# Kernel tuning notes

Hardware: AMD Instinct MI355X
Metric: run time of the kernel (lower is better)

The kernel has to match this reference:

```python
import jax, jax.numpy as jnp
import numpy as np

B, N, C = 8, 8192, 64
P, K = 2048, 16
C_IN = 2 * C + 6   # 134: concat(diff, center) of (feat ++ xyz)
H1, H2 = 64, 128
EPS = 1e-5


def setup_inputs() -> dict:
    key = jax.random.key(0)
    ks = jax.random.split(key, 16)
    inp = {
        "xyz": jax.random.normal(ks[0], (B, N, 3), dtype=jnp.float32),
        "feat": jax.random.normal(ks[1], (B, C, N), dtype=jnp.float32),
        # SharedMLP layer 1: 1x1 conv + BN(eval) + ReLU
        "W1": jax.random.normal(ks[2], (H1, C_IN), dtype=jnp.float32) * (1.0 / np.sqrt(C_IN)),
        "b1": jnp.zeros((H1,), dtype=jnp.float32),
        "g1": jax.random.uniform(ks[3], (H1,), minval=0.5, maxval=1.5, dtype=jnp.float32),
        "be1": jax.random.normal(ks[4], (H1,), dtype=jnp.float32) * 0.1,
        "m1": jax.random.normal(ks[5], (H1,), dtype=jnp.float32) * 0.1,
        "v1": jax.random.uniform(ks[6], (H1,), minval=0.5, maxval=1.5, dtype=jnp.float32),
        # SharedMLP layer 2
        "W2": jax.random.normal(ks[7], (H2, H1), dtype=jnp.float32) * (1.0 / np.sqrt(H1)),
        "b2": jnp.zeros((H2,), dtype=jnp.float32),
        "g2": jax.random.uniform(ks[8], (H2,), minval=0.5, maxval=1.5, dtype=jnp.float32),
        "be2": jax.random.normal(ks[9], (H2,), dtype=jnp.float32) * 0.1,
        "m2": jax.random.normal(ks[10], (H2,), dtype=jnp.float32) * 0.1,
        "v2": jax.random.uniform(ks[11], (H2,), minval=0.5, maxval=1.5, dtype=jnp.float32),
        "npoints": P,
    }
    return inp


def _mlp_layer(x, W, b, g, be, m, v):
    # x: [b,p,k,cin] -> 1x1 conv (einsum) + eval-mode BN + ReLU
    y = jnp.einsum("bpkc,oc->bpko", x, W) + b
    y = g * (y - m) * jax.lax.rsqrt(v + EPS) + be
    return jax.nn.relu(y)


def reference(xyz, feat, W1, b1, g1, be1, m1, v1, W2, b2, g2, be2, m2, v2, npoints):
    p = npoints
    # Range sampling: take first p points
    new_xyz = xyz[:, :p]                       # [b,p,3]
    feat_t = jnp.swapaxes(feat, 1, 2)          # [b,n,c]
    feat_x = jnp.concatenate([feat_t, xyz], axis=-1)   # [b,n,c+3] (use_xyz)
    new_feat_x = feat_x[:, :p]                 # [b,p,c+3]
    # KNN via squared euclidean distance, expanded form to avoid [b,p,n,3]
    sq_q = jnp.sum(new_xyz * new_xyz, axis=-1)           # [b,p]
    sq_r = jnp.sum(xyz * xyz, axis=-1)                   # [b,n]
    dots = jnp.einsum("bpd,bnd->bpn", new_xyz, xyz)      # [b,p,n]
    d2 = sq_q[:, :, None] + sq_r[:, None, :] - 2.0 * dots
    _, idx = jax.lax.top_k(-d2, K)             # [b,p,k] nearest (ascending dist)
    # Gather neighbor features: [b,p,k,c+3]
    knn_feat = jax.vmap(lambda f, i: f[i])(feat_x, idx)
    tiled = jnp.broadcast_to(new_feat_x[:, :, None, :], knn_feat.shape)
    edge = jnp.concatenate([knn_feat - tiled, tiled], axis=-1)  # [b,p,k,2c+6]
    h = _mlp_layer(edge, W1, b1, g1, be1, m1, v1)
    h = _mlp_layer(h, W2, b2, g2, be2, m2, v2)              # [b,p,k,H2]
    new_feat = jnp.swapaxes(jnp.max(h, axis=2), 1, 2)       # [b,H2,p]
    sample_idx = jnp.broadcast_to(jnp.arange(p, dtype=jnp.int32), (xyz.shape[0], p))
    return new_xyz, new_feat, sample_idx
```

## Files before the change

### kernel.cpp

```cpp
#include <hip/hip_runtime.h>
#include <hip/hip_bf16.h>

#define BB 8
#define NN 8192
#define CC 64
#define PP 2048
#define KK 16
#define H1 64
#define H2 128
#define K1PAD 160
#define K2PAD 72

typedef float  f32x4 __attribute__((ext_vector_type(4)));
typedef short  s16x8 __attribute__((ext_vector_type(8)));

#define OFF_FXT   0u
#define OFF_PTS4  17825792u
#define OFF_KNN   19922944u
#define OFF_W1P   20971520u
#define OFF_W2P   20992000u
#define OFF_C1    21010432u
#define OFF_C2    21010688u

#define FLTMAX 3.402823466e+38f

static __device__ __forceinline__ unsigned short bf16b(float v) {
    __hip_bfloat16 h = __float2bfloat16(v);
    return *reinterpret_cast<unsigned short*>(&h);
}
static __device__ __forceinline__ unsigned pk2(float a, float b) {
    return ((unsigned)bf16b(b) << 16) | (unsigned)bf16b(a);
}
#define LDS_FENCE() asm volatile("s_waitcnt lgkmcnt(0)" ::: "memory")

__global__ void k0_weights(const float* __restrict__ W1, const float* __restrict__ b1,
                           const float* __restrict__ g1, const float* __restrict__ be1,
                           const float* __restrict__ m1, const float* __restrict__ v1,
                           const float* __restrict__ W2, const float* __restrict__ b2,
                           const float* __restrict__ g2, const float* __restrict__ be2,
                           const float* __restrict__ m2, const float* __restrict__ v2,
                           unsigned short* __restrict__ w1p, unsigned short* __restrict__ w2p,
                           float* __restrict__ c1, float* __restrict__ c2) {
    int i = blockIdx.x * 256 + threadIdx.x;
    if (i < 64 * K1PAD) {
        int n = i / K1PAD, c = i - n * K1PAD;
        float s = g1[n] * rsqrtf(v1[n] + 1e-5f);
        float val = 0.f;
        if (c < 67)                 val = W1[n * 134 + c] * s;
        else if (c >= 72 && c < 139) val = W1[n * 134 + (c - 5)] * s;
        w1p[i] = bf16b(val);
    }
    int j = i - 64 * K1PAD;
    if (j >= 0 && j < 128 * K2PAD) {
        int o = j / K2PAD, k = j - o * K2PAD;
        float s = g2[o] * rsqrtf(v2[o] + 1e-5f);
        w2p[j] = bf16b((k < 64) ? W2[o * 64 + k] * s : 0.f);
    }
    int l = i - (64 * K1PAD + 128 * K2PAD);
    if (l >= 0 && l < 64) {
        float s = g1[l] * rsqrtf(v1[l] + 1e-5f);
        c1[l] = s * (b1[l] - m1[l]) + be1[l];
    }
    int p = l - 64;
    if (p >= 0 && p < 128) {
        float s = g2[p] * rsqrtf(v2[p] + 1e-5f);
        c2[p] = s * (b2[p] - m2[p]) + be2[p];
    }
}

__global__ __launch_bounds__(512) void k1_prep(const float* __restrict__ xyz,
                                               const float* __restrict__ feat,
                                               float* __restrict__ fxt,
                                               float4* __restrict__ pts4,
                                               float* __restrict__ out0,
                                               float* __restrict__ out2) {
    __shared__ float tile[68][65];
    int b  = blockIdx.x >> 7;
    int n0 = (blockIdx.x & 127) * 64;
    int tx = threadIdx.x & 63, ty = threadIdx.x >> 6;
    for (int c = ty; c < 68; c += 8) {
        float v;
        if (c < 64)       v = feat[((size_t)b * 64 + c) * NN + n0 + tx];
        else if (c < 67)  v = xyz[((size_t)b * NN + n0 + tx) * 3 + (c - 64)];
        else              v = 0.f;
        tile[c][tx] = v;
    }
    __syncthreads();
    size_t base = ((size_t)b * NN + n0) * 68;
    for (int e = threadIdx.x; e < 64 * 68; e += 512) {
        int nl = e / 68, c = e - nl * 68;
        fxt[base + e] = tile[c][nl];
    }
    if (threadIdx.x < 64) {
        int n = n0 + threadIdx.x;
        float x = tile[64][threadIdx.x], y = tile[65][threadIdx.x], z = tile[66][threadIdx.x];
        pts4[(size_t)b * NN + n] = make_float4(x, y, z, x * x + y * y + z * z);
        if (n0 < PP) out2[b * PP + n] = (float)n;
    }
    if (n0 < PP) {
        for (int e = threadIdx.x; e < 64 * 3; e += 512) {
            int nl = e / 3, d = e - nl * 3;
            out0[((size_t)b * PP + n0 + nl) * 3 + d] = tile[64 + d][nl];
        }
    }
}

__global__ __launch_bounds__(1024, 2) void k2_knn(const float4* __restrict__ pts4,
                                                  int* __restrict__ knn) {
    __shared__ float4 stage[8192];
    __shared__ float2 scratch[16][2][64];
    int lane = threadIdx.x & 63;
    int wv   = threadIdx.x >> 6;
    int b    = blockIdx.x >> 5;
    int q0   = (blockIdx.x & 31) * 64 + wv * 4;
    size_t pb = (size_t)b * NN;

    float4 qc = make_float4(0.f, 0.f, 0.f, 0.f);
    if (lane < 4) qc = pts4[pb + q0 + lane];
    float qx2 = -2.f * qc.x, qy2 = -2.f * qc.y, qz2 = -2.f * qc.z;
    float bx[4], by[4], bz[4];
#pragma unroll
    for (int q = 0; q < 4; ++q) {
        bx[q] = __shfl(qx2, q); by[q] = __shfl(qy2, q); bz[q] = __shfl(qz2, q);
    }

#pragma unroll
    for (int i = 0; i < 8; ++i) {
        int p = i * 1024 + threadIdx.x;
        float4 v = pts4[pb + p];
        int r = p >> 6, c = p & 63;
        stage[(r << 6) | ((c + (r >> 1)) & 63)] = v;
    }
    __syncthreads();

    float m[4];
#pragma unroll
    for (int q = 0; q < 4; ++q) m[q] = FLTMAX;
#pragma unroll
    for (int rr = 0; rr < 2; ++rr) {
        int rowbase = (2 * lane + rr) << 6;
#pragma unroll
        for (int j8 = 0; j8 < 8; ++j8) {
            float4 cc[8];
#pragma unroll
            for (int i = 0; i < 8; ++i)
                cc[i] = stage[rowbase | ((j8 * 8 + i + lane) & 63)];
#pragma unroll
            for (int q = 0; q < 4; ++q) {
                float x = bx[q], y = by[q], z = bz[q];
#pragma unroll
                for (int i = 0; i < 8; i += 2) {
                    float e0 = fmaf(z, cc[i].z, fmaf(y, cc[i].y, fmaf(x, cc[i].x, cc[i].w)));
                    float e1 = fmaf(z, cc[i+1].z, fmaf(y, cc[i+1].y, fmaf(x, cc[i+1].x, cc[i+1].w)));
                    m[q] = fminf(fminf(m[q], e0), e1);
                }
            }
        }
    }

    float sv0 = m[0], sv1 = m[1], sv2 = m[2], sv3 = m[3];
#pragma unroll
    for (int k = 2; k <= 64; k <<= 1) {
#pragma unroll
        for (int j = k >> 1; j > 0; j >>= 1) {
            bool keepMin = (((lane & k) == 0) == ((lane & j) == 0));
            float p0 = __shfl_xor(sv0, j, 64);
            float p1 = __shfl_xor(sv1, j, 64);
            float p2 = __shfl_xor(sv2, j, 64);
            float p3 = __shfl_xor(sv3, j, 64);
            sv0 = keepMin ? fminf(sv0, p0) : fmaxf(sv0, p0);
            sv1 = keepMin ? fminf(sv1, p1) : fmaxf(sv1, p1);
            sv2 = keepMin ? fminf(sv2, p2) : fmaxf(sv2, p2);
            sv3 = keepMin ? fminf(sv3, p3) : fmaxf(sv3, p3);
        }
    }
    float T[4];
    T[0] = __shfl(sv0, 15, 64); T[1] = __shfl(sv1, 15, 64);
    T[2] = __shfl(sv2, 15, 64); T[3] = __shfl(sv3, 15, 64);

    unsigned long long below = (lane == 63) ? 0x7FFFFFFFFFFFFFFFull
                                            : ((1ull << lane) - 1ull);
#pragma unroll
    for (int pr = 0; pr < 4; pr += 2) {
        int Ms[2];
#pragma unroll
        for (int u = 0; u < 2; ++u) {
            int q = pr + u;
            float x = bx[q], y = by[q], z = bz[q], tq = T[q];
            unsigned long long rm = __ballot(m[q] <= tq);
            int cnt = 0;
            while (rm) {
                int sl = __ffsll((long long)rm) - 1; rm &= rm - 1;
                int phys = (lane + sl) & 63;
                float4 c0 = stage[((2 * sl) << 6) | phys];
                float4 c1 = stage[((2 * sl + 1) << 6) | phys];
                float e0 = fmaf(z, c0.z, fmaf(y, c0.y, fmaf(x, c0.x, c0.w)));
                float e1 = fmaf(z, c1.z, fmaf(y, c1.y, fmaf(x, c1.x, c1.w)));
                unsigned long long b0 = __ballot(e0 <= tq);
                if (e0 <= tq) {
                    int pos = cnt + __popcll(b0 & below);
                    if (pos < 64)
                        scratch[wv][u][pos] = make_float2(e0, __int_as_float(sl * 128 + lane));
                }
                cnt += __popcll(b0);
                unsigned long long b1 = __ballot(e1 <= tq);
                if (e1 <= tq) {
                    int pos = cnt + __popcll(b1 & below);
                    if (pos < 64)
                        scratch[wv][u][pos] = make_float2(e1, __int_as_float(sl * 128 + 64 + lane));
                }
                cnt += __popcll(b1);
            }
            Ms[u] = min(cnt, 64);
        }
        LDS_FENCE();
#pragma unroll
        for (int u = 0; u < 2; ++u) {
            int M = Ms[u];
            float2 own = scratch[wv][u][lane];
            float di = own.x; int ni = __float_as_int(own.y);
            int rank = 0;
            const float2* buf = &scratch[wv][u][0];
#pragma unroll 4
            for (int j = 0; j < M; ++j) {
                float2 e = buf[j];
                int nj = __float_as_int(e.y);
                rank += (e.x < di || (e.x == di && nj < ni)) ? 1 : 0;
            }
            if (lane < M && rank < 16)
                knn[((size_t)(b * PP + q0 + pr + u)) * KK + rank] = ni;
        }
        LDS_FENCE();
    }
}

__global__ __launch_bounds__(256, 2) void k3_mlp(const float* __restrict__ fxt,
                                                 const int* __restrict__ knn,
                                                 const unsigned short* __restrict__ w1p,
                                                 const unsigned short* __restrict__ w2p,
                                                 const float* __restrict__ c1,
                                                 const float* __restrict__ c2,
                                                 float* __restrict__ out1) {
    __shared__ __align__(16) char smem[4 * 5632];
    __shared__ float otile[16][132];
    __shared__ __align__(16) unsigned short w1lds[64 * 168];
    int lane = threadIdx.x & 63;
    int wv   = threadIdx.x >> 6;
    int b    = blockIdx.x & 7;
    int qg   = blockIdx.x >> 3;
    int qbase = qg * 16;
    char* seg = smem + wv * 5632;
    float4* sh_t4 = (float4*)(seg + 5120);
    unsigned* sh_tbd = (unsigned*)(seg + 5392);
    unsigned short* h1l = (unsigned short*)(seg);
    const float4* fx4 = (const float4*)fxt;

    int col = lane & 15, quad = lane >> 4;
    int r = lane >> 2, s = lane & 3;

    {
        const unsigned* src = (const unsigned*)w1p;
        unsigned* dst = (unsigned*)w1lds;
        for (int t = threadIdx.x; t < 5120; t += 256) {
            int row = t / 80, c = t - row * 80;
            dst[row * 84 + c] = src[t];
        }
    }

    s16x8 w2f[2][8];
#pragma unroll
    for (int ks = 0; ks < 2; ++ks)
#pragma unroll
        for (int nt = 0; nt < 8; ++nt)
            w2f[ks][nt] = *(const s16x8*)(w2p + (nt * 16 + col) * K2PAD + ks * 32 + quad * 8);
    float c1v[4], c2v[8];
#pragma unroll
    for (int nt = 0; nt < 4; ++nt) c1v[nt] = c1[nt * 16 + col];
#pragma unroll
    for (int nt = 0; nt < 8; ++nt) c2v[nt] = c2[nt * 16 + col];

    int idxAll = knn[((size_t)(b * PP + qbase + wv * 4)) * KK + lane];

    __syncthreads();

    float4 cc[2][5];
    float4 tv[2];

#define PREFETCH(buf, qi_) {                                                  \
        int q_ = qbase + wv * 4 + (qi_);                                      \
        tv[buf] = make_float4(0.f, 0.f, 0.f, 0.f);                            \
        if (lane < 17) tv[buf] = fx4[((size_t)b * NN + q_) * 17 + lane];      \
        int nidx_ = __shfl(idxAll, (qi_) * 16 + r, 64);                       \
        const float4* rowp_ = fx4 + ((size_t)b * NN + nidx_) * 17;            \
        cc[buf][0] = rowp_[s];      cc[buf][1] = rowp_[4 + s];                \
        cc[buf][2] = rowp_[8 + s];  cc[buf][3] = rowp_[12 + s];               \
        cc[buf][4] = rowp_[16]; }

    PREFETCH(0, 0);

#pragma unroll
    for (int qi = 0; qi < 4; ++qi) {
        int cur = qi & 1, nxt = cur ^ 1;
        if (lane < 17) {
            float4 v = tv[cur];
            sh_t4[lane] = v;
            sh_tbd[lane * 2]     = pk2(v.x, v.y);
            sh_tbd[lane * 2 + 1] = pk2(v.z, v.w);
        }
        LDS_FENCE();
        char* erow = seg + r * 320;
#pragma unroll
        for (int j = 0; j < 4; ++j) {
            int c4 = j * 4 + s;
            float4 v = cc[cur][j], t = sh_t4[c4];
            *(unsigned*)(erow + c4 * 8)     = pk2(v.x - t.x, v.y - t.y);
            *(unsigned*)(erow + c4 * 8 + 4) = pk2(v.z - t.z, v.w - t.w);
        }
        if (s == 0) {
            float4 v = cc[cur][4], t = sh_t4[16];
            *(unsigned*)(erow + 128) = pk2(v.x - t.x, v.y - t.y);
            *(unsigned*)(erow + 132) = pk2(v.z - t.z, v.w - t.w);
        }
        for (int j = s; j < 34; j += 4)
            *(unsigned*)(erow + 144 + j * 4) = sh_tbd[j];
#pragma unroll
        for (int i = lane; i < 192; i += 64) {
            int rr = i / 12, jj = i - rr * 12;
            int dw = (jj < 2) ? (34 + jj) : (68 + jj);
            *(unsigned*)(seg + rr * 320 + dw * 4) = 0u;
        }
        if (qi < 3) PREFETCH(nxt, qi + 1);
        LDS_FENCE();
        f32x4 acc1[4];
#pragma unroll
        for (int nt = 0; nt < 4; ++nt) acc1[nt] = (f32x4){0.f, 0.f, 0.f, 0.f};
#pragma unroll
        for (int ks = 0; ks < 5; ++ks) {
            s16x8 a = *(const s16x8*)(seg + col * 320 + ks * 64 + quad * 16);
#pragma unroll
            for (int nt = 0; nt < 4; ++nt) {
                s16x8 bf = *(const s16x8*)(w1lds + (nt * 16 + col) * 168 + ks * 32 + quad * 8);
                acc1[nt] = __builtin_amdgcn_mfma_f32_16x16x32_bf16(a, bf, acc1[nt], 0, 0, 0);
            }
        }
#pragma unroll
        for (int nt = 0; nt < 4; ++nt) {
#pragma unroll
            for (int rr = 0; rr < 4; ++rr) {
                float y = fmaxf(acc1[nt][rr] + c1v[nt], 0.f);
                h1l[(quad * 4 + rr) * K2PAD + nt * 16 + col] = bf16b(y);
            }
        }
        {
            int rr = lane >> 2, dd = lane & 3;
            *(unsigned*)(seg + rr * 144 + 128 + dd * 4) = 0u;
        }
        LDS_FENCE();
        f32x4 acc2[8];
#pragma unroll
        for (int nt = 0; nt < 8; ++nt) acc2[nt] = (f32x4){0.f, 0.f, 0.f, 0.f};
#pragma unroll
        for (int ks = 0; ks < 2; ++ks) {
            s16x8 a = *(const s16x8*)(seg + col * 144 + ks * 64 + quad * 16);
#pragma unroll
            for (int nt = 0; nt < 8; ++nt)
                acc2[nt] = __builtin_amdgcn_mfma_f32_16x16x32_bf16(a, w2f[ks][nt], acc2[nt], 0, 0, 0);
        }
#pragma unroll
        for (int nt = 0; nt < 8; ++nt) {
            float m0 = fmaxf(fmaxf(acc2[nt][0], acc2[nt][1]), fmaxf(acc2[nt][2], acc2[nt][3]));
            m0 = m0 + c2v[nt];
            m0 = fmaxf(m0, 0.f);
            m0 = fmaxf(m0, __shfl_xor(m0, 16, 64));
            m0 = fmaxf(m0, __shfl_xor(m0, 32, 64));
            if (quad == 0)
                otile[wv * 4 + qi][nt * 16 + col] = m0;
        }
        LDS_FENCE();
    }
    __syncthreads();
    for (int i = threadIdx.x; i < H2 * 16; i += 256) {
        int ch = i >> 4, q = i & 15;
        out1[((size_t)(b * H2 + ch)) * PP + qbase + q] = otile[q][ch];
    }
#undef PREFETCH
}

extern "C" void kernel_launch(void* const* d_in, const int* in_sizes, int n_in,
                              void* d_out, int out_size, void* d_ws, size_t ws_size,
                              hipStream_t stream) {
    const float* xyz  = (const float*)d_in[0];
    const float* feat = (const float*)d_in[1];
    const float* W1   = (const float*)d_in[2];
    const float* b1   = (const float*)d_in[3];
    const float* g1   = (const float*)d_in[4];
    const float* be1  = (const float*)d_in[5];
    const float* m1   = (const float*)d_in[6];
    const float* v1   = (const float*)d_in[7];
    const float* W2   = (const float*)d_in[8];
    const float* b2   = (const float*)d_in[9];
    const float* g2   = (const float*)d_in[10];
    const float* be2  = (const float*)d_in[11];
    const float* m2   = (const float*)d_in[12];
    const float* v2   = (const float*)d_in[13];

    char* ws = (char*)d_ws;
    float*          fxt  = (float*)(ws + OFF_FXT);
    float4*         pts4 = (float4*)(ws + OFF_PTS4);
    int*            knn  = (int*)(ws + OFF_KNN);
    unsigned short* w1p  = (unsigned short*)(ws + OFF_W1P);
    unsigned short* w2p  = (unsigned short*)(ws + OFF_W2P);
    float*          c1   = (float*)(ws + OFF_C1);
    float*          c2   = (float*)(ws + OFF_C2);

    float* out0 = (float*)d_out;
    float* out1 = out0 + (size_t)BB * PP * 3;
    float* out2 = out1 + (size_t)BB * H2 * PP;

    hipLaunchKernelGGL(k0_weights, dim3(77), dim3(256), 0, stream,
                       W1, b1, g1, be1, m1, v1, W2, b2, g2, be2, m2, v2,
                       w1p, w2p, c1, c2);
    hipLaunchKernelGGL(k1_prep, dim3(1024), dim3(512), 0, stream,
                       xyz, feat, fxt, pts4, out0, out2);
    hipLaunchKernelGGL(k2_knn, dim3(256), dim3(1024), 0, stream, pts4, knn);
    hipLaunchKernelGGL(k3_mlp, dim3(1024), dim3(256), 0, stream,
                       fxt, knn, w1p, w2p, c1, c2, out1);
}
```

Measured before the change: 169.1 us.

## Split KNN candidate rows across wave pairs and fuse weight prep into prep kernel

The KNN kernel now has each pair of waves share 8 queries instead of each wave owning 4. Each wave scans half the candidate rows, the two partial top-16 thresholds are merged through LDS, and survivors are appended to a shared buffer of up to 128 entries using LDS atomics. Ranking is then split between the two waves. The weight-folding kernel is merged into the prep kernel as one extra block, removing a launch. The change adds block-wide barriers and atomic contention. The tighter combined threshold or the 128-entry cap could also change behaviour with many ties.

Result: slower. 210.9 us (+24.7%).

```diff
diff --git a/kernel.cpp b/kernel.cpp
--- a/kernel.cpp
+++ b/kernel.cpp
@@ -33,47 +33,47 @@
 }
 #define LDS_FENCE() asm volatile("s_waitcnt lgkmcnt(0)" ::: "memory")
 
-__global__ void k0_weights(const float* __restrict__ W1, const float* __restrict__ b1,
-                           const float* __restrict__ g1, const float* __restrict__ be1,
-                           const float* __restrict__ m1, const float* __restrict__ v1,
-                           const float* __restrict__ W2, const float* __restrict__ b2,
-                           const float* __restrict__ g2, const float* __restrict__ be2,
-                           const float* __restrict__ m2, const float* __restrict__ v2,
-                           unsigned short* __restrict__ w1p, unsigned short* __restrict__ w2p,
-                           float* __restrict__ c1, float* __restrict__ c2) {
-    int i = blockIdx.x * 256 + threadIdx.x;
-    if (i < 64 * K1PAD) {
-        int n = i / K1PAD, c = i - n * K1PAD;
-        float s = g1[n] * rsqrtf(v1[n] + 1e-5f);
-        float val = 0.f;
-        if (c < 67)                 val = W1[n * 134 + c] * s;
-        else if (c >= 72 && c < 139) val = W1[n * 134 + (c - 5)] * s;
-        w1p[i] = bf16b(val);
-    }
-    int j = i - 64 * K1PAD;
-    if (j >= 0 && j < 128 * K2PAD) {
-        int o = j / K2PAD, k = j - o * K2PAD;
-        float s = g2[o] * rsqrtf(v2[o] + 1e-5f);
-        w2p[j] = bf16b((k < 64) ? W2[o * 64 + k] * s : 0.f);
-    }
-    int l = i - (64 * K1PAD + 128 * K2PAD);
-    if (l >= 0 && l < 64) {
-        float s = g1[l] * rsqrtf(v1[l] + 1e-5f);
-        c1[l] = s * (b1[l] - m1[l]) + be1[l];
-    }
-    int p = l - 64;
-    if (p >= 0 && p < 128) {
-        float s = g2[p] * rsqrtf(v2[p] + 1e-5f);
-        c2[p] = s * (b2[p] - m2[p]) + be2[p];
-    }
-}
-
 __global__ __launch_bounds__(512) void k1_prep(const float* __restrict__ xyz,
                                                const float* __restrict__ feat,
+                                               const float* __restrict__ W1, const float* __restrict__ b1,
+                                               const float* __restrict__ g1, const float* __restrict__ be1,
+                                               const float* __restrict__ m1, const float* __restrict__ v1,
+                                               const float* __restrict__ W2, const float* __restrict__ b2,
+                                               const float* __restrict__ g2, const float* __restrict__ be2,
+                                               const float* __restrict__ m2, const float* __restrict__ v2,
                                                float* __restrict__ fxt,
                                                float4* __restrict__ pts4,
                                                float* __restrict__ out0,
-                                               float* __restrict__ out2) {
+                                               float* __restrict__ out2,
+                                               unsigned short* __restrict__ w1p,
+                                               unsigned short* __restrict__ w2p,
+                                               float* __restrict__ c1, float* __restrict__ c2) {
+    if (blockIdx.x >= 1024) {
+        for (int i = threadIdx.x; i < 19648; i += 512) {
+            if (i < 64 * K1PAD) {
+                int n = i / K1PAD, c = i - n * K1PAD;
+                float s = g1[n] * rsqrtf(v1[n] + 1e-5f);
+                float val = 0.f;
+                if (c < 67)                  val = W1[n * 134 + c] * s;
+                else if (c >= 72 && c < 139) val = W1[n * 134 + (c - 5)] * s;
+                w1p[i] = bf16b(val);
+            } else if (i < 19456) {
+                int j = i - 10240;
+                int o = j / K2PAD, k = j - o * K2PAD;
+                float s = g2[o] * rsqrtf(v2[o] + 1e-5f);
+                w2p[j] = bf16b((k < 64) ? W2[o * 64 + k] * s : 0.f);
+            } else if (i < 19520) {
+                int l = i - 19456;
+                float s = g1[l] * rsqrtf(v1[l] + 1e-5f);
+                c1[l] = s * (b1[l] - m1[l]) + be1[l];
+            } else {
+                int p = i - 19520;
+                float s = g2[p] * rsqrtf(v2[p] + 1e-5f);
+                c2[p] = s * (b2[p] - m2[p]) + be2[p];
+            }
+        }
+        return;
+    }
     __shared__ float tile[68][65];
     int b  = blockIdx.x >> 7;
     int n0 = (blockIdx.x & 127) * 64;
@@ -105,22 +105,28 @@
     }
 }
 
-__global__ __launch_bounds__(1024, 2) void k2_knn(const float4* __restrict__ pts4,
+__global__ __launch_bounds__(1024, 4) void k2_knn(const float4* __restrict__ pts4,
                                                   int* __restrict__ knn) {
     __shared__ float4 stage[8192];
-    __shared__ float2 scratch[16][2][64];
+    __shared__ float2 scratch[8][2][128];
+    __shared__ float  Tbuf[16][8];
+    __shared__ int    cnt[8][2];
     int lane = threadIdx.x & 63;
     int wv   = threadIdx.x >> 6;
+    int pair = wv & 7;
+    int half = wv >> 3;
     int b    = blockIdx.x >> 5;
-    int q0   = (blockIdx.x & 31) * 64 + wv * 4;
+    int q0   = (blockIdx.x & 31) * 64 + pair * 8;
     size_t pb = (size_t)b * NN;
 
+    if (threadIdx.x < 16) cnt[threadIdx.x >> 1][threadIdx.x & 1] = 0;
+
     float4 qc = make_float4(0.f, 0.f, 0.f, 0.f);
-    if (lane < 4) qc = pts4[pb + q0 + lane];
+    if (lane < 8) qc = pts4[pb + q0 + lane];
     float qx2 = -2.f * qc.x, qy2 = -2.f * qc.y, qz2 = -2.f * qc.z;
-    float bx[4], by[4], bz[4];
-#pragma unroll
-    for (int q = 0; q < 4; ++q) {
+    float bx[8], by[8], bz[8];
+#pragma unroll
+    for (int q = 0; q < 8; ++q) {
         bx[q] = __shfl(qx2, q); by[q] = __shfl(qy2, q); bz[q] = __shfl(qz2, q);
     }
 
@@ -133,104 +139,118 @@
     }
     __syncthreads();
 
-    float m[4];
-#pragma unroll
-    for (int q = 0; q < 4; ++q) m[q] = FLTMAX;
-#pragma unroll
-    for (int rr = 0; rr < 2; ++rr) {
-        int rowbase = (2 * lane + rr) << 6;
-#pragma unroll
-        for (int j8 = 0; j8 < 8; ++j8) {
-            float4 cc[8];
-#pragma unroll
-            for (int i = 0; i < 8; ++i)
-                cc[i] = stage[rowbase | ((j8 * 8 + i + lane) & 63)];
-#pragma unroll
-            for (int q = 0; q < 4; ++q) {
-                float x = bx[q], y = by[q], z = bz[q];
-#pragma unroll
-                for (int i = 0; i < 8; i += 2) {
-                    float e0 = fmaf(z, cc[i].z, fmaf(y, cc[i].y, fmaf(x, cc[i].x, cc[i].w)));
-                    float e1 = fmaf(z, cc[i+1].z, fmaf(y, cc[i+1].y, fmaf(x, cc[i+1].x, cc[i+1].w)));
-                    m[q] = fminf(fminf(m[q], e0), e1);
-                }
-            }
-        }
-    }
-
-    float sv0 = m[0], sv1 = m[1], sv2 = m[2], sv3 = m[3];
+    int row = half * 64 + lane;
+    int rowbase = row << 6;
+    float m[8];
+#pragma unroll
+    for (int q = 0; q < 8; ++q) m[q] = FLTMAX;
+#pragma unroll
+    for (int j8 = 0; j8 < 8; ++j8) {
+        float4 cc[8];
+#pragma unroll
+        for (int i = 0; i < 8; ++i)
+            cc[i] = stage[rowbase | ((j8 * 8 + i + lane) & 63)];
+#pragma unroll
+        for (int q = 0; q < 8; ++q) {
+            float x = bx[q], y = by[q], z = bz[q];
+#pragma unroll
+            for (int i = 0; i < 8; i += 2) {
+                float e0 = fmaf(z, cc[i].z, fmaf(y, cc[i].y, fmaf(x, cc[i].x, cc[i].w)));
+                float e1 = fmaf(z, cc[i+1].z, fmaf(y, cc[i+1].y, fmaf(x, cc[i+1].x, cc[i+1].w)));
+                m[q] = fminf(fminf(m[q], e0), e1);
+            }
+        }
+    }
+
+    float sv[8];
+#pragma unroll
+    for (int q = 0; q < 8; ++q) sv[q] = m[q];
 #pragma unroll
     for (int k = 2; k <= 64; k <<= 1) {
 #pragma unroll
         for (int j = k >> 1; j > 0; j >>= 1) {
             bool keepMin = (((lane & k) == 0) == ((lane & j) == 0));
-            float p0 = __shfl_xor(sv0, j, 64);
-            float p1 = __shfl_xor(sv1, j, 64);
-            float p2 = __shfl_xor(sv2, j, 64);
-            float p3 = __shfl_xor(sv3, j, 64);
-            sv0 = keepMin ? fminf(sv0, p0) : fmaxf(sv0, p0);
-            sv1 = keepMin ? fminf(sv1, p1) : fmaxf(sv1, p1);
-            sv2 = keepMin ? fminf(sv2, p2) : fmaxf(sv2, p2);
-            sv3 = keepMin ? fminf(sv3, p3) : fmaxf(sv3, p3);
-        }
-    }
-    float T[4];
-    T[0] = __shfl(sv0, 15, 64); T[1] = __shfl(sv1, 15, 64);
-    T[2] = __shfl(sv2, 15, 64); T[3] = __shfl(sv3, 15, 64);
+#pragma unroll
+            for (int q = 0; q < 8; ++q) {
+                float p = __shfl_xor(sv[q], j, 64);
+                sv[q] = keepMin ? fminf(sv[q], p) : fmaxf(sv[q], p);
+            }
+        }
+    }
+    if (lane == 0) {
+#pragma unroll
+        for (int q = 0; q < 8; ++q) Tbuf[wv][q] = 0.f;
+    }
+    float Town[8];
+#pragma unroll
+    for (int q = 0; q < 8; ++q) Town[q] = __shfl(sv[q], 15, 64);
+    if (lane == 0) {
+#pragma unroll
+        for (int q = 0; q < 8; ++q) Tbuf[wv][q] = Town[q];
+    }
+    __syncthreads();
+    float T[8];
+    unsigned long long rm[8];
+#pragma unroll
+    for (int q = 0; q < 8; ++q) {
+        T[q] = fminf(Tbuf[pair][q], Tbuf[pair + 8][q]);
+        rm[q] = __ballot(m[q] <= T[q]);
+    }
 
     unsigned long long below = (lane == 63) ? 0x7FFFFFFFFFFFFFFFull
                                             : ((1ull << lane) - 1ull);
-#pragma unroll
-    for (int pr = 0; pr < 4; pr += 2) {
-        int Ms[2];
+#pragma unroll 1
+    for (int pr = 0; pr < 8; pr += 2) {
 #pragma unroll
         for (int u = 0; u < 2; ++u) {
             int q = pr + u;
             float x = bx[q], y = by[q], z = bz[q], tq = T[q];
-            unsigned long long rm = __ballot(m[q] <= tq);
-            int cnt = 0;
-            while (rm) {
-                int sl = __ffsll((long long)rm) - 1; rm &= rm - 1;
+            unsigned long long r = rm[q];
+            while (r) {
+                int sl = __ffsll((long long)r) - 1; r &= r - 1;
+                int rw = half * 64 + sl;
                 int phys = (lane + sl) & 63;
-                float4 c0 = stage[((2 * sl) << 6) | phys];
-                float4 c1 = stage[((2 * sl + 1) << 6) | phys];
-                float e0 = fmaf(z, c0.z, fmaf(y, c0.y, fmaf(x, c0.x, c0.w)));
-                float e1 = fmaf(z, c1.z, fmaf(y, c1.y, fmaf(x, c1.x, c1.w)));
-                unsigned long long b0 = __ballot(e0 <= tq);
-                if (e0 <= tq) {
-                    int pos = cnt + __popcll(b0 & below);
-                    if (pos < 64)
-                        scratch[wv][u][pos] = make_float2(e0, __int_as_float(sl * 128 + lane));
+                float4 c = stage[(rw << 6) | phys];
+                float e = fmaf(z, c.z, fmaf(y, c.y, fmaf(x, c.x, c.w)));
+                int n = (rw << 6) | ((phys - (rw >> 1)) & 63);
+                unsigned long long bal = __ballot(e <= tq);
+                if (bal) {
+                    int src = __ffsll((long long)bal) - 1;
+                    int nsurv = __popcll(bal);
+                    int base = 0;
+                    if (lane == src) base = atomicAdd(&cnt[pair][u], nsurv);
+                    base = __shfl(base, src, 64);
+                    if (e <= tq) {
+                        int pos = base + __popcll(bal & below);
+                        if (pos < 128)
+                            scratch[pair][u][pos] = make_float2(e, __int_as_float(n));
+                    }
                 }
-                cnt += __popcll(b0);
-                unsigned long long b1 = __ballot(e1 <= tq);
-                if (e1 <= tq) {
-                    int pos = cnt + __popcll(b1 & below);
-                    if (pos < 64)
-                        scratch[wv][u][pos] = make_float2(e1, __int_as_float(sl * 128 + 64 + lane));
-                }
-                cnt += __popcll(b1);
-            }
-            Ms[u] = min(cnt, 64);
-        }
-        LDS_FENCE();
-#pragma unroll
-        for (int u = 0; u < 2; ++u) {
-            int M = Ms[u];
-            float2 own = scratch[wv][u][lane];
-            float di = own.x; int ni = __float_as_int(own.y);
-            int rank = 0;
-            const float2* buf = &scratch[wv][u][0];
+            }
+        }
+        __syncthreads();
+        {
+            int u = half;
+            int M = min(cnt[pair][u], 128);
+            float2 own0 = scratch[pair][u][lane];
+            float2 own1 = scratch[pair][u][lane + 64];
+            float d0 = (lane < M) ? own0.x : FLTMAX;      int n0 = __float_as_int(own0.y);
+            float d1 = (lane + 64 < M) ? own1.x : FLTMAX; int n1 = __float_as_int(own1.y);
+            int r0 = 0, r1 = 0;
+            const float2* buf = &scratch[pair][u][0];
 #pragma unroll 4
             for (int j = 0; j < M; ++j) {
                 float2 e = buf[j];
                 int nj = __float_as_int(e.y);
-                rank += (e.x < di || (e.x == di && nj < ni)) ? 1 : 0;
-            }
-            if (lane < M && rank < 16)
-                knn[((size_t)(b * PP + q0 + pr + u)) * KK + rank] = ni;
-        }
-        LDS_FENCE();
+                r0 += (e.x < d0 || (e.x == d0 && nj < n0)) ? 1 : 0;
+                r1 += (e.x < d1 || (e.x == d1 && nj < n1)) ? 1 : 0;
+            }
+            size_t obase = ((size_t)(b * PP + q0 + pr + u)) * KK;
+            if (lane < M && r0 < 16)      knn[obase + r0] = n0;
+            if (lane + 64 < M && r1 < 16) knn[obase + r1] = n1;
+            if (lane == 0) cnt[pair][u] = 0;
+        }
+        __syncthreads();
     }
 }
 
@@ -417,11 +437,9 @@
     float* out1 = out0 + (size_t)BB * PP * 3;
     float* out2 = out1 + (size_t)BB * H2 * PP;
 
-    hipLaunchKernelGGL(k0_weights, dim3(77), dim3(256), 0, stream,
-                       W1, b1, g1, be1, m1, v1, W2, b2, g2, be2, m2, v2,
-                       w1p, w2p, c1, c2);
-    hipLaunchKernelGGL(k1_prep, dim3(1024), dim3(512), 0, stream,
-                       xyz, feat, fxt, pts4, out0, out2);
+    hipLaunchKernelGGL(k1_prep, dim3(1025), dim3(512), 0, stream,
+                       xyz, feat, W1, b1, g1, be1, m1, v1, W2, b2, g2, be2, m2, v2,
+                       fxt, pts4, out0, out2, w1p, w2p, c1, c2);
     hipLaunchKernelGGL(k2_knn, dim3(256), dim3(1024), 0, stream, pts4, knn);
     hipLaunchKernelGGL(k3_mlp, dim3(1024), dim3(256), 0, stream,
                        fxt, knn, w1p, w2p, c1, c2, out1);
```
